# Kernel optimization log

Measured on AMD Instinct MI355X. Metric: run time of the kernel, lower is better.

Reference implementation:

```python
import jax, jax.numpy as jnp
import numpy as np

N_HEADS = 4
M = 16            # n_points (neighbors kept per voxel)
DIST = 4          # manhattan distance threshold
D_MODEL = 128
D_FFN = 256
D_CHL = 64
GRID = 96         # spatial_shape per axis
LN_EPS = 1e-5
BN_EPS = 1e-3


def setup_inputs() -> dict:
    key = jax.random.key(0)
    ks = jax.random.split(key, 24)
    N = 8192
    w = lambda k, s: jax.random.normal(k, s, jnp.float32) * 0.02
    z = lambda d: jnp.zeros((d,), jnp.float32)
    o = lambda d: jnp.ones((d,), jnp.float32)
    return {
        "features": jax.random.normal(ks[0], (N, D_CHL), jnp.float32),
        "coords": jax.random.randint(ks[1], (N, 3), 0, GRID, jnp.int32),
        "pe_w1": w(ks[2], (3, D_MODEL // 2)), "pe_b1": z(D_MODEL // 2),
        "pe_w2": w(ks[3], (D_MODEL // 2, D_MODEL)), "pe_b2": z(D_MODEL),
        "in_w": w(ks[4], (D_CHL, D_MODEL)), "in_b": z(D_MODEL),
        "q_w": w(ks[5], (D_MODEL, D_MODEL)), "q_b": z(D_MODEL),
        "k_w": w(ks[6], (D_MODEL, D_MODEL)), "k_b": z(D_MODEL),
        "v_w": w(ks[7], (D_MODEL, D_MODEL)), "v_b": z(D_MODEL),
        "o_w": w(ks[8], (D_MODEL, D_MODEL)), "o_b": z(D_MODEL),
        "n1_g": o(D_MODEL), "n1_b": z(D_MODEL),
        "l1_w": w(ks[9], (D_MODEL, D_FFN)), "l1_b": z(D_FFN),
        "l2_w": w(ks[10], (D_FFN, D_MODEL)), "l2_b": z(D_MODEL),
        "n3_g": o(D_MODEL), "n3_b": z(D_MODEL),
        "fu_w": w(ks[11], (D_MODEL + D_CHL, D_CHL)), "fu_b": z(D_CHL),
        "bn_g": o(D_CHL), "bn_b": z(D_CHL),
    }


def _layernorm(x, g, b):
    mu = jnp.mean(x, -1, keepdims=True)
    var = jnp.mean(jnp.square(x - mu), -1, keepdims=True)
    return (x - mu) * jax.lax.rsqrt(var + LN_EPS) * g + b


def reference(features, coords, pe_w1, pe_b1, pe_w2, pe_b2, in_w, in_b,
              q_w, q_b, k_w, k_b, v_w, v_b, o_w, o_b, n1_g, n1_b,
              l1_w, l1_b, l2_w, l2_b, n3_g, n3_b, fu_w, fu_b, bn_g, bn_b):
    N = features.shape[0]
    hd = D_MODEL // N_HEADS
    ci = coords.astype(jnp.float32)
    # input projection + dynamic learnable positional encoding
    src = features @ in_w + in_b
    vc = ci / (GRID - 1.0)
    src = src + (jax.nn.relu(vc @ pe_w1 + pe_b1) @ pe_w2 + pe_b2)
    # pairwise manhattan distances; accumulate per coordinate to avoid [N,N,3]
    dist = jnp.zeros((N, N), jnp.float32)
    for d in range(3):
        dist = dist + jnp.abs(ci[:, d, None] - ci[None, :, d])
    dist = jnp.where(dist <= DIST, dist, jnp.inf)
    neg_top, idx = jax.lax.top_k(-dist, M)          # [N, M]
    valid = neg_top != -jnp.inf
    # gather neighbor features; invalid slots are zero (as in torch)
    nb = jnp.where(valid[:, :, None], src[jnp.where(valid, idx, 0)], 0.0)  # [N,M,D]
    # cross-attention: query is neighbor 0 (self). NOTE: faithful raw .view
    # reshape of [N,M,D] -> [N,H,M,hd] (interleaves neighbor/head axes as torch does)
    q = (nb[:, :1] @ q_w + q_b).reshape(N, N_HEADS, 1, hd)
    k = (nb @ k_w + k_b).reshape(N, N_HEADS, M, hd)
    v = (nb @ v_w + v_b).reshape(N, N_HEADS, M, hd)
    scores = jnp.einsum('nhqd,nhkd->nhqk', q, k) / jnp.sqrt(jnp.float32(D_MODEL))
    attn = jax.nn.softmax(scores, axis=-1)
    head_out = jnp.einsum('nhqk,nhkd->nhqd', attn, v).reshape(N, D_MODEL)
    out = head_out @ o_w + o_b
    tgt = _layernorm(src + out, n1_g, n1_b)
    # FFN
    tgt2 = jax.nn.relu(tgt @ l1_w + l1_b) @ l2_w + l2_b
    tgt = _layernorm(tgt + tgt2, n3_g, n3_b)
    # EnhancedFusion: concat -> linear -> batchnorm (train-mode stats) -> relu
    fused = jnp.concatenate([features, tgt], axis=1) @ fu_w + fu_b
    mu = jnp.mean(fused, 0)
    var = jnp.var(fused, 0)
    fused = (fused - mu) * jax.lax.rsqrt(var + BN_EPS) * bn_g + bn_b
    return jax.nn.relu(fused)
```

## Files before the change

### kernel.cpp

```cpp
#include <hip/hip_runtime.h>

#define DEVFN __device__ __forceinline__

DEVFN float relu(float x) { return x < 0.f ? 0.f : x; }

typedef _Float16 h2 __attribute__((ext_vector_type(2)));
DEVFN float dot2(unsigned a, unsigned b, float c) {
    return __builtin_amdgcn_fdot2(__builtin_bit_cast(h2, a),
                                  __builtin_bit_cast(h2, b), c, false);
}
DEVFN unsigned pack2(float x, float y) {
    h2 h; h.x = (_Float16)x; h.y = (_Float16)y;
    return __builtin_bit_cast(unsigned, h);
}

#define OFF_Q   0
#define OFF_K   8192
#define OFF_V   16384
#define OFF_O   24576
#define OFF_L1  32768
#define OFF_L2  49152
#define OFF_IN  65536
#define OFF_PE  69632
#define OFF_FU  73728
#define PACKED_TOTAL 79872

__global__ __launch_bounds__(256) void k0_pack(
    const float* __restrict__ q_w, const float* __restrict__ k_w,
    const float* __restrict__ v_w, const float* __restrict__ o_w,
    const float* __restrict__ l1_w, const float* __restrict__ l2_w,
    const float* __restrict__ in_w, const float* __restrict__ pe_w2,
    const float* __restrict__ fu_w, unsigned* __restrict__ dst)
{
    const int gid = blockIdx.x * 256 + threadIdx.x;
    const int stride = gridDim.x * 256;
    auto packmat = [&](const float* s, int K, int C, unsigned* d) {
        const int kp2 = K / 2;
        const int n = kp2 * C;
        const int c4 = C * 4;
        for (int i = gid; i < n; i += stride) {
            int kp4 = i / c4;
            int rem = i - kp4 * c4;
            int c = rem >> 2, ki = rem & 3;
            int kp = kp4 * 4 + ki;
            d[i] = pack2(s[(2 * kp) * C + c], s[(2 * kp + 1) * C + c]);
        }
    };
    packmat(q_w, 128, 128, dst + OFF_Q);
    packmat(k_w, 128, 128, dst + OFF_K);
    packmat(v_w, 128, 128, dst + OFF_V);
    packmat(o_w, 128, 128, dst + OFF_O);
    packmat(l1_w, 128, 256, dst + OFF_L1);
    packmat(l2_w, 256, 128, dst + OFF_L2);
    packmat(in_w, 64, 128, dst + OFF_IN);
    packmat(pe_w2, 64, 128, dst + OFF_PE);
    packmat(fu_w, 192, 64, dst + OFF_FU);
}

__global__ __launch_bounds__(256, 4) void ka_pre_cst(
    const float* __restrict__ features, const int* __restrict__ coords,
    const float* __restrict__ pe_w1, const float* __restrict__ pe_b1,
    const float* __restrict__ pe_b2,
    const float* __restrict__ in_b,
    const unsigned* __restrict__ wH,
    float* __restrict__ src,
    float* __restrict__ qs, float* __restrict__ ks, float* __restrict__ vs,
    int* __restrict__ nbr, float* __restrict__ bnAcc, int N)
{
    __shared__ __align__(16) float S[1024];
    __shared__ __align__(16) unsigned SH[512];
    __shared__ __align__(16) unsigned FHp[256];
    __shared__ __align__(16) unsigned HHp[256];
    __shared__ int   sC[24];
    __shared__ int cnt[16];
    __shared__ int lst[16 * 64];
    __shared__ int outL[256];

    const int tid = threadIdx.x;
    const int bx = blockIdx.x;
    const int role_nbr = (bx % 3) == 2;

    if (role_nbr) {
        const int nb = bx / 3;
        const int q0 = nb * 16;
        if (nb == 0 && tid < 128) bnAcc[tid] = 0.f;
        if (tid < 16) cnt[tid] = 0;
        outL[tid] = -1;
        __syncthreads();
        int qx[16], qy[16], qz[16];
#pragma unroll
        for (int q = 0; q < 16; ++q) {
            qx[q] = coords[(q0 + q) * 3 + 0];
            qy[q] = coords[(q0 + q) * 3 + 1];
            qz[q] = coords[(q0 + q) * 3 + 2];
        }
        for (int cd = tid; cd < N; cd += 256) {
            int cx = coords[cd * 3 + 0];
            int cy = coords[cd * 3 + 1];
            int cz = coords[cd * 3 + 2];
#pragma unroll
            for (int q = 0; q < 16; ++q) {
                int dx = cx - qx[q]; dx = dx < 0 ? -dx : dx;
                int dy = cy - qy[q]; dy = dy < 0 ? -dy : dy;
                int dz = cz - qz[q]; dz = dz < 0 ? -dz : dz;
                int d = dx + dy + dz;
                if (d <= 4) {
                    int s = atomicAdd(&cnt[q], 1);
                    if (s < 64) lst[q * 64 + s] = (d << 13) | cd;
                }
            }
        }
        __syncthreads();
        {
            const int q = tid >> 4, t = tid & 15;
            int n = cnt[q]; if (n > 64) n = 64;
            for (int e = t; e < n; e += 16) {
                int key = lst[q * 64 + e];
                int rank = 0;
                for (int j = 0; j < n; ++j) rank += (lst[q * 64 + j] < key) ? 1 : 0;
                if (rank < 16) outL[q * 16 + rank] = key & 8191;
            }
        }
        __syncthreads();
        {
            const int q = tid >> 4, t = tid & 15;
            nbr[(q0 + q) * 16 + t] = outL[q * 16 + t];
        }
        return;
    }

    const int sb = (bx / 3) * 2 + (bx % 3);
    const int r0 = sb * 8;
    if (tid < 24) sC[tid] = coords[r0 * 3 + tid];
    if (tid < 256) {
        float2 f = *(const float2*)(features + r0 * 64 + tid * 2);
        FHp[tid] = pack2(f.x, f.y);
    }
    __syncthreads();
    if (tid < 256) {
        int r = tid >> 5, t2 = (tid & 31) * 2;
        float v0 = sC[r * 3 + 0] * (1.f / 95.f);
        float v1 = sC[r * 3 + 1] * (1.f / 95.f);
        float v2 = sC[r * 3 + 2] * (1.f / 95.f);
        float h0 = v0 * pe_w1[t2] + v1 * pe_w1[64 + t2] + v2 * pe_w1[128 + t2] + pe_b1[t2];
        float h1 = v0 * pe_w1[t2 + 1] + v1 * pe_w1[64 + t2 + 1] + v2 * pe_w1[128 + t2 + 1] + pe_b1[t2 + 1];
        HHp[tid] = pack2(relu(h0), relu(h1));
    }
    __syncthreads();
    const int c = tid & 127, rh = tid >> 7;
    {
        const unsigned* inH = wH + OFF_IN + c * 4;
        const unsigned* peH = wH + OFF_PE + c * 4;
        float acc[4];
        const float base = in_b[c] + pe_b2[c];
#pragma unroll
        for (int r = 0; r < 4; ++r) acc[r] = base;
        for (int kp4 = 0; kp4 < 8; ++kp4) {
            uint4 wi = *(const uint4*)(inH + kp4 * 512);
            uint4 wp = *(const uint4*)(peH + kp4 * 512);
#pragma unroll
            for (int r = 0; r < 4; ++r) {
                const int rr = rh * 4 + r;
                uint4 f = *(const uint4*)(&FHp[rr * 32 + kp4 * 4]);
                uint4 h = *(const uint4*)(&HHp[rr * 32 + kp4 * 4]);
                acc[r] = dot2(f.x, wi.x, acc[r]); acc[r] = dot2(f.y, wi.y, acc[r]);
                acc[r] = dot2(f.z, wi.z, acc[r]); acc[r] = dot2(f.w, wi.w, acc[r]);
                acc[r] = dot2(h.x, wp.x, acc[r]); acc[r] = dot2(h.y, wp.y, acc[r]);
                acc[r] = dot2(h.z, wp.z, acc[r]); acc[r] = dot2(h.w, wp.w, acc[r]);
            }
        }
#pragma unroll
        for (int r = 0; r < 4; ++r) {
            src[(r0 + rh * 4 + r) * 128 + c] = acc[r];
            S[(rh * 4 + r) * 128 + c] = acc[r];
        }
    }
    __syncthreads();
    for (int i = tid; i < 512; i += 256) {
        float2 s = *(const float2*)(&S[i * 2]);
        SH[i] = pack2(s.x, s.y);
    }
    __syncthreads();
    {
        const unsigned* qH = wH + OFF_Q + c * 4;
        const unsigned* kH = wH + OFF_K + c * 4;
        const unsigned* vH = wH + OFF_V + c * 4;
        float aq[4], ak[4], av[4];
#pragma unroll
        for (int r = 0; r < 4; ++r) { aq[r] = 0.f; ak[r] = 0.f; av[r] = 0.f; }
        for (int kp4 = 0; kp4 < 16; ++kp4) {
            uint4 wq = *(const uint4*)(qH + kp4 * 512);
            uint4 wk = *(const uint4*)(kH + kp4 * 512);
            uint4 wv = *(const uint4*)(vH + kp4 * 512);
#pragma unroll
            for (int r = 0; r < 4; ++r) {
                uint4 s4 = *(const uint4*)(&SH[(rh * 4 + r) * 64 + kp4 * 4]);
                aq[r] = dot2(s4.x, wq.x, aq[r]); aq[r] = dot2(s4.y, wq.y, aq[r]);
                aq[r] = dot2(s4.z, wq.z, aq[r]); aq[r] = dot2(s4.w, wq.w, aq[r]);
                ak[r] = dot2(s4.x, wk.x, ak[r]); ak[r] = dot2(s4.y, wk.y, ak[r]);
                ak[r] = dot2(s4.z, wk.z, ak[r]); ak[r] = dot2(s4.w, wk.w, ak[r]);
                av[r] = dot2(s4.x, wv.x, av[r]); av[r] = dot2(s4.y, wv.y, av[r]);
                av[r] = dot2(s4.z, wv.z, av[r]); av[r] = dot2(s4.w, wv.w, av[r]);
            }
        }
#pragma unroll
        for (int r = 0; r < 4; ++r) {
            qs[(r0 + rh * 4 + r) * 128 + c] = aq[r];
            ks[(r0 + rh * 4 + r) * 128 + c] = ak[r];
            vs[(r0 + rh * 4 + r) * 128 + c] = av[r];
        }
    }
}

DEVFN void ln_rows8_pack(float* Cb, unsigned* CHp, const float* __restrict__ g,
                         const float* __restrict__ b, int tid)
{
    const int r = tid >> 5, l = tid & 31;
    float x[4]; float s = 0.f, s2 = 0.f;
#pragma unroll
    for (int i = 0; i < 4; ++i) {
        x[i] = Cb[r * 128 + l * 4 + i];
        s += x[i]; s2 += x[i] * x[i];
    }
#pragma unroll
    for (int o = 1; o < 32; o <<= 1) { s += __shfl_xor(s, o); s2 += __shfl_xor(s2, o); }
    float mu = s * (1.f / 128.f);
    float var = s2 * (1.f / 128.f) - mu * mu;
    float rstd = rsqrtf(var + 1e-5f);
    float y[4];
#pragma unroll
    for (int i = 0; i < 4; ++i) {
        int cc = l * 4 + i;
        y[i] = (x[i] - mu) * rstd * g[cc] + b[cc];
        Cb[r * 128 + cc] = y[i];
    }
    CHp[r * 64 + l * 2]     = pack2(y[0], y[1]);
    CHp[r * 64 + l * 2 + 1] = pack2(y[2], y[3]);
}

__global__ __launch_bounds__(256, 4) void k4_main_cst(
    const float* __restrict__ features, const float* __restrict__ src,
    const float* __restrict__ qs, const float* __restrict__ ks, const float* __restrict__ vs,
    const int* __restrict__ nbr,
    const float* __restrict__ q_b, const float* __restrict__ k_b,
    const float* __restrict__ v_b,
    const unsigned* __restrict__ wH,
    const float* __restrict__ o_b,
    const float* __restrict__ n1_g, const float* __restrict__ n1_b,
    const float* __restrict__ l1_b,
    const float* __restrict__ l2_b,
    const float* __restrict__ n3_g, const float* __restrict__ n3_b,
    const float* __restrict__ fu_b,
    float* __restrict__ fused, float* __restrict__ bnSum, float* __restrict__ bnSq)
{
    __shared__ __align__(16) float A[1024];
    __shared__ __align__(16) float C[1024];
    __shared__ __align__(16) float Q[1024];
    __shared__ __align__(16) float SC[512];
    __shared__ __align__(16) unsigned BtH[512];
    __shared__ __align__(16) unsigned CH[512];
    __shared__ __align__(16) unsigned FH[256];
    __shared__ __align__(16) _Float16 Hh[2048];
    __shared__ __align__(16) float bK[128], bV[128];
    __shared__ int idxL[128];
    const int tid = threadIdx.x;
    const int r0 = blockIdx.x * 8;

    for (int i = tid; i < 1024; i += 256) A[i] = src[r0 * 128 + i];
    if (tid < 256) {
        float2 f = *(const float2*)(features + r0 * 64 + tid * 2);
        FH[tid] = pack2(f.x, f.y);
    }
    if (tid < 128) {
        idxL[tid] = nbr[r0 * 16 + tid];
        bK[tid] = k_b[tid]; bV[tid] = v_b[tid];
    }
    __syncthreads();
    {
        int r = tid >> 5, cg = tid & 31;
        int i0 = idxL[r * 16];
        float4 qv = make_float4(0.f, 0.f, 0.f, 0.f);
        if (i0 >= 0) qv = *(const float4*)(qs + i0 * 128 + cg * 4);
        float4 qb = *(const float4*)(q_b + cg * 4);
        qv.x += qb.x; qv.y += qb.y; qv.z += qb.z; qv.w += qb.w;
        *(float4*)(&Q[r * 128 + cg * 4]) = qv;
    }
    __syncthreads();

    const int ar = tid >> 5, ah = (tid >> 3) & 3, ag = tid & 7;
    {
        const int ch = ag & 3;
        float sbias = 0.f;
#pragma unroll
        for (int c4 = 0; c4 < 8; ++c4) {
            float4 qv = *(const float4*)(&Q[ar * 128 + ah * 32 + c4 * 4]);
            float4 kb = *(const float4*)(&bK[ch * 32 + c4 * 4]);
            sbias += qv.x * kb.x + qv.y * kb.y + qv.z * kb.z + qv.w * kb.w;
        }
#pragma unroll
        for (int jj = 0; jj < 2; ++jj) {
            int j = ag + jj * 8;
            int j4 = j >> 2;
            int id = idxL[ar * 16 + ah * 4 + j4];
            float s = 0.f;
            if (id >= 0) {
#pragma unroll
                for (int c4 = 0; c4 < 8; ++c4) {
                    float4 qv = *(const float4*)(&Q[ar * 128 + ah * 32 + c4 * 4]);
                    float4 kv = *(const float4*)(ks + id * 128 + ch * 32 + c4 * 4);
                    s += qv.x * kv.x + qv.y * kv.y + qv.z * kv.z + qv.w * kv.w;
                }
            }
            SC[ar * 64 + ah * 16 + j] = (s + sbias) * 0.08838834764831845f;
        }
    }
    __syncthreads();

    {
        float p[16];
        float mx = -3.4e38f;
#pragma unroll
        for (int j = 0; j < 16; ++j) { p[j] = SC[ar * 64 + ah * 16 + j]; mx = fmaxf(mx, p[j]); }
        float sum = 0.f;
#pragma unroll
        for (int j = 0; j < 16; ++j) { p[j] = __expf(p[j] - mx); sum += p[j]; }
        float inv = 1.f / sum;
        float4 acc = make_float4(0.f, 0.f, 0.f, 0.f);
#pragma unroll
        for (int j = 0; j < 16; ++j) {
            int j4 = j >> 2, ch = j & 3;
            int id = idxL[ar * 16 + ah * 4 + j4];
            float w = p[j] * inv;
            if (id >= 0) {
                float4 vv = *(const float4*)(vs + id * 128 + ch * 32 + ag * 4);
                acc.x += w * vv.x; acc.y += w * vv.y;
                acc.z += w * vv.z; acc.w += w * vv.w;
            }
        }
        float4 vb = *(const float4*)(&bV[ah * 32 + ag * 4]);
        acc.x += vb.x; acc.y += vb.y; acc.z += vb.z; acc.w += vb.w;
        BtH[ar * 64 + ah * 16 + ag * 2]     = pack2(acc.x, acc.y);
        BtH[ar * 64 + ah * 16 + ag * 2 + 1] = pack2(acc.z, acc.w);
    }
    __syncthreads();

    {
        const int c = tid & 127, rh = tid >> 7;
        const unsigned* oH = wH + OFF_O + c * 4;
        float acc[4];
#pragma unroll
        for (int r = 0; r < 4; ++r) acc[r] = 0.f;
        for (int kp4 = 0; kp4 < 16; ++kp4) {
            uint4 w = *(const uint4*)(oH + kp4 * 512);
#pragma unroll
            for (int r = 0; r < 4; ++r) {
                uint4 t = *(const uint4*)(&BtH[(rh * 4 + r) * 64 + kp4 * 4]);
                acc[r] = dot2(t.x, w.x, acc[r]); acc[r] = dot2(t.y, w.y, acc[r]);
                acc[r] = dot2(t.z, w.z, acc[r]); acc[r] = dot2(t.w, w.w, acc[r]);
            }
        }
        const float ob = o_b[c];
#pragma unroll
        for (int r = 0; r < 4; ++r) {
            const int rr = rh * 4 + r;
            C[rr * 128 + c] = A[rr * 128 + c] + ob + acc[r];
        }
    }
    __syncthreads();
    ln_rows8_pack(C, CH, n1_g, n1_b, tid);
    __syncthreads();

    {
        const int f = tid;
        const unsigned* l1H = wH + OFF_L1 + f * 4;
        float acc[8];
#pragma unroll
        for (int r = 0; r < 8; ++r) acc[r] = 0.f;
        for (int kp4 = 0; kp4 < 16; ++kp4) {
            uint4 w = *(const uint4*)(l1H + kp4 * 1024);
#pragma unroll
            for (int r = 0; r < 8; ++r) {
                uint4 t = *(const uint4*)(&CH[r * 64 + kp4 * 4]);
                acc[r] = dot2(t.x, w.x, acc[r]); acc[r] = dot2(t.y, w.y, acc[r]);
                acc[r] = dot2(t.z, w.z, acc[r]); acc[r] = dot2(t.w, w.w, acc[r]);
            }
        }
        const float bb = l1_b[f];
#pragma unroll
        for (int r = 0; r < 8; ++r) Hh[r * 256 + f] = (_Float16)relu(acc[r] + bb);
    }
    __syncthreads();
    {
    }

    {
        const int c = tid & 127, rh = tid >> 7;
        const unsigned* l2H = wH + OFF_L2 + c * 4;
        const unsigned* HhU = (const unsigned*)Hh;
        float acc[4];
#pragma unroll
        for (int r = 0; r < 4; ++r) acc[r] = 0.f;
        for (int kp4 = 0; kp4 < 32; ++kp4) {
            uint4 w = *(const uint4*)(l2H + kp4 * 512);
#pragma unroll
            for (int r = 0; r < 4; ++r) {
                uint4 t = *(const uint4*)(&HhU[(rh * 4 + r) * 128 + kp4 * 4]);
                acc[r] = dot2(t.x, w.x, acc[r]); acc[r] = dot2(t.y, w.y, acc[r]);
                acc[r] = dot2(t.z, w.z, acc[r]); acc[r] = dot2(t.w, w.w, acc[r]);
            }
        }
        const float lb = l2_b[c];
#pragma unroll
        for (int r = 0; r < 4; ++r) {
            const int rr = rh * 4 + r;
            C[rr * 128 + c] += lb + acc[r];
        }
    }
    __syncthreads();
    ln_rows8_pack(C, CH, n3_g, n3_b, tid);
    __syncthreads();

    {
        const int c = tid & 63, rg = tid >> 6;
        const unsigned* fuH = wH + OFF_FU + c * 4;
        float acc[2];
        const float fb = fu_b[c];
#pragma unroll
        for (int r = 0; r < 2; ++r) acc[r] = fb;
        for (int kp4 = 0; kp4 < 8; ++kp4) {
            uint4 w = *(const uint4*)(fuH + kp4 * 256);
#pragma unroll
            for (int r = 0; r < 2; ++r) {
                uint4 t = *(const uint4*)(&FH[(rg * 2 + r) * 32 + kp4 * 4]);
                acc[r] = dot2(t.x, w.x, acc[r]); acc[r] = dot2(t.y, w.y, acc[r]);
                acc[r] = dot2(t.z, w.z, acc[r]); acc[r] = dot2(t.w, w.w, acc[r]);
            }
        }
        for (int kp4 = 0; kp4 < 16; ++kp4) {
            uint4 w = *(const uint4*)(fuH + (8 + kp4) * 256);
#pragma unroll
            for (int r = 0; r < 2; ++r) {
                uint4 t = *(const uint4*)(&CH[(rg * 2 + r) * 64 + kp4 * 4]);
                acc[r] = dot2(t.x, w.x, acc[r]); acc[r] = dot2(t.y, w.y, acc[r]);
                acc[r] = dot2(t.z, w.z, acc[r]); acc[r] = dot2(t.w, w.w, acc[r]);
            }
        }
#pragma unroll
        for (int r = 0; r < 2; ++r) {
            int row = rg * 2 + r;
            float v = acc[r];
            fused[(r0 + row) * 64 + c] = v;
            A[row * 64 + c] = v;
        }
    }
    __syncthreads();
    if (tid < 64) {
        float s = 0.f, s2 = 0.f;
#pragma unroll
        for (int r = 0; r < 8; ++r) { float x = A[r * 64 + tid]; s += x; s2 += x * x; }
        atomicAdd(&bnSum[tid], s);
        atomicAdd(&bnSq[tid], s2);
    }
}

__global__ __launch_bounds__(256) void k5_bn_cst(
    const float* __restrict__ fused, const float* __restrict__ bnSum,
    const float* __restrict__ bnSq,
    const float* __restrict__ g, const float* __restrict__ b,
    float* __restrict__ out, int N)
{
    const int total = N * 64;
    const float invN = 1.f / (float)N;
    for (int i = blockIdx.x * 256 + threadIdx.x; i < total; i += gridDim.x * 256) {
        int c = i & 63;
        float mu = bnSum[c] * invN;
        float var = bnSq[c] * invN - mu * mu;
        float x = fused[i];
        float y = (x - mu) * rsqrtf(var + 1e-3f) * g[c] + b[c];
        out[i] = relu(y);
    }
}

extern "C" void kernel_launch(void* const* d_in, const int* in_sizes, int n_in,
                              void* d_out, int out_size, void* d_ws, size_t ws_size,
                              hipStream_t stream)
{
    const float* features = (const float*)d_in[0];
    const int*   coords   = (const int*)d_in[1];
    const float* pe_w1 = (const float*)d_in[2];
    const float* pe_b1 = (const float*)d_in[3];
    const float* pe_w2 = (const float*)d_in[4];
    const float* pe_b2 = (const float*)d_in[5];
    const float* in_w  = (const float*)d_in[6];
    const float* in_b  = (const float*)d_in[7];
    const float* q_w   = (const float*)d_in[8];
    const float* q_b   = (const float*)d_in[9];
    const float* k_w   = (const float*)d_in[10];
    const float* k_b   = (const float*)d_in[11];
    const float* v_w   = (const float*)d_in[12];
    const float* v_b   = (const float*)d_in[13];
    const float* o_w   = (const float*)d_in[14];
    const float* o_b   = (const float*)d_in[15];
    const float* n1_g  = (const float*)d_in[16];
    const float* n1_b  = (const float*)d_in[17];
    const float* l1_w  = (const float*)d_in[18];
    const float* l1_b  = (const float*)d_in[19];
    const float* l2_w  = (const float*)d_in[20];
    const float* l2_b  = (const float*)d_in[21];
    const float* n3_g  = (const float*)d_in[22];
    const float* n3_b  = (const float*)d_in[23];
    const float* fu_w  = (const float*)d_in[24];
    const float* fu_b  = (const float*)d_in[25];
    const float* bn_g  = (const float*)d_in[26];
    const float* bn_b  = (const float*)d_in[27];

    const int N = in_sizes[0] / 64;

    float* src   = (float*)d_ws;
    float* qs    = src + (size_t)N * 128;
    float* ks    = qs  + (size_t)N * 128;
    float* vs    = ks  + (size_t)N * 128;
    float* fused = vs  + (size_t)N * 128;
    int*   nbr    = (int*)(fused + (size_t)N * 64);
    float* bnSum  = (float*)(nbr + (size_t)N * 16);
    float* bnSq   = bnSum + 64;
    unsigned* wH  = (unsigned*)(bnSq + 64);

    k0_pack<<<64, 256, 0, stream>>>(q_w, k_w, v_w, o_w, l1_w, l2_w,
                                    in_w, pe_w2, fu_w, wH);
    ka_pre_cst<<<N / 8 + N / 16, 256, 0, stream>>>(features, coords,
                                                   pe_w1, pe_b1, pe_b2, in_b,
                                                   wH,
                                                   src, qs, ks, vs, nbr, bnSum, N);
    k4_main_cst<<<N / 8, 256, 0, stream>>>(features, src, qs, ks, vs, nbr,
                                           q_b, k_b, v_b, wH, o_b, n1_g, n1_b,
                                           l1_b, l2_b, n3_g, n3_b,
                                           fu_b, fused, bnSum, bnSq);
    k5_bn_cst<<<512, 256, 0, stream>>>(fused, bnSum, bnSq, bn_g, bn_b,
                                       (float*)d_out, N);
}
```

Baseline: 207.6 us.

## Fuse all stages into one cooperative persistent kernel with grid syncs

Replaces the four launches (weight pack, pre-projection/neighbor search, main attention+FFN, batchnorm) with one cooperative kernel of N/16 blocks. Each block handles two 8-row tiles, separated by grid.sync barriers. The src activations and fused outputs stay in registers across phases instead of going to global memory, and shared memory is a union across phases. This removes launch overhead and intermediate global traffic, at the cost of grid-wide barriers and 512 blocks that must all be co-resident. If the cooperative launch fails, the old kernels run instead.

```diff
diff --git a/kernel.cpp b/kernel.cpp
--- a/kernel.cpp
+++ b/kernel.cpp
@@ -1,4 +1,7 @@
 #include <hip/hip_runtime.h>
+#include <hip/hip_cooperative_groups.h>
+
+namespace cg = cooperative_groups;
 
 #define DEVFN __device__ __forceinline__
 
@@ -23,7 +26,481 @@
 #define OFF_IN  65536
 #define OFF_PE  69632
 #define OFF_FU  73728
-#define PACKED_TOTAL 79872
+
+struct MegaParams {
+    const float* features; const int* coords;
+    const float* pe_w1; const float* pe_b1; const float* pe_w2; const float* pe_b2;
+    const float* in_w;  const float* in_b;
+    const float* q_w;   const float* q_b;
+    const float* k_w;   const float* k_b;
+    const float* v_w;   const float* v_b;
+    const float* o_w;   const float* o_b;
+    const float* n1_g;  const float* n1_b;
+    const float* l1_w;  const float* l1_b;
+    const float* l2_w;  const float* l2_b;
+    const float* n3_g;  const float* n3_b;
+    const float* fu_w;  const float* fu_b;
+    const float* bn_g;  const float* bn_b;
+    float* qs; float* ks; float* vs; int* nbr;
+    float* bnSum; float* bnSq; unsigned* wH;
+    float* out; int N;
+};
+
+__global__ __launch_bounds__(256, 2) void mega_cst(MegaParams P)
+{
+    cg::grid_group grid = cg::this_grid();
+    const int tid = threadIdx.x;
+    const int bx = blockIdx.x;
+    const int gid = bx * 256 + tid;
+
+    __shared__ union SU {
+        struct {
+            float S[1024];
+            unsigned SH[512];
+            unsigned FHp[256];
+            unsigned HHp[256];
+            int sC[24];
+            int cnt[8];
+            int lst[8 * 64];
+            int outL[128];
+        } ka;
+        struct {
+            float A[1024]; float C[1024]; float Q[1024]; float SC[512];
+            unsigned BtH[512]; unsigned CH[512]; unsigned FH[256];
+            _Float16 Hh[2048]; float bK[128]; float bV[128]; int idxL[128];
+        } k4;
+    } U;
+
+    {
+        const int stride = gridDim.x * 256;
+        auto packmat = [&](const float* s, int K, int C, unsigned* d) {
+            const int kp2 = K / 2;
+            const int n = kp2 * C;
+            const int c4 = C * 4;
+            for (int i = gid; i < n; i += stride) {
+                int kp4 = i / c4;
+                int rem = i - kp4 * c4;
+                int c = rem >> 2, ki = rem & 3;
+                int kp = kp4 * 4 + ki;
+                d[i] = pack2(s[(2 * kp) * C + c], s[(2 * kp + 1) * C + c]);
+            }
+        };
+        packmat(P.q_w, 128, 128, P.wH + OFF_Q);
+        packmat(P.k_w, 128, 128, P.wH + OFF_K);
+        packmat(P.v_w, 128, 128, P.wH + OFF_V);
+        packmat(P.o_w, 128, 128, P.wH + OFF_O);
+        packmat(P.l1_w, 128, 256, P.wH + OFF_L1);
+        packmat(P.l2_w, 256, 128, P.wH + OFF_L2);
+        packmat(P.in_w, 64, 128, P.wH + OFF_IN);
+        packmat(P.pe_w2, 64, 128, P.wH + OFF_PE);
+        packmat(P.fu_w, 192, 64, P.wH + OFF_FU);
+        if (gid < 128) P.bnSum[gid] = 0.f;
+    }
+    __threadfence();
+    grid.sync();
+
+    float accS[2][4];
+
+#pragma unroll
+    for (int t = 0; t < 2; ++t) {
+        const int r0 = (bx + t * 512) * 8;
+        __syncthreads();
+
+        if (tid < 24) U.ka.sC[tid] = P.coords[r0 * 3 + tid];
+        {
+            float2 f = *(const float2*)(P.features + r0 * 64 + tid * 2);
+            U.ka.FHp[tid] = pack2(f.x, f.y);
+        }
+        __syncthreads();
+        {
+            int r = tid >> 5, t2 = (tid & 31) * 2;
+            float v0 = U.ka.sC[r * 3 + 0] * (1.f / 95.f);
+            float v1 = U.ka.sC[r * 3 + 1] * (1.f / 95.f);
+            float v2 = U.ka.sC[r * 3 + 2] * (1.f / 95.f);
+            float h0 = v0 * P.pe_w1[t2] + v1 * P.pe_w1[64 + t2] + v2 * P.pe_w1[128 + t2] + P.pe_b1[t2];
+            float h1 = v0 * P.pe_w1[t2 + 1] + v1 * P.pe_w1[64 + t2 + 1] + v2 * P.pe_w1[128 + t2 + 1] + P.pe_b1[t2 + 1];
+            U.ka.HHp[tid] = pack2(relu(h0), relu(h1));
+        }
+        __syncthreads();
+        const int c = tid & 127, rh = tid >> 7;
+        {
+            const unsigned* inH = P.wH + OFF_IN + c * 4;
+            const unsigned* peH = P.wH + OFF_PE + c * 4;
+            float acc[4];
+            const float base = P.in_b[c] + P.pe_b2[c];
+#pragma unroll
+            for (int r = 0; r < 4; ++r) acc[r] = base;
+            for (int kp4 = 0; kp4 < 8; ++kp4) {
+                uint4 wi = *(const uint4*)(inH + kp4 * 512);
+                uint4 wp = *(const uint4*)(peH + kp4 * 512);
+#pragma unroll
+                for (int r = 0; r < 4; ++r) {
+                    const int rr = rh * 4 + r;
+                    uint4 f = *(const uint4*)(&U.ka.FHp[rr * 32 + kp4 * 4]);
+                    uint4 h = *(const uint4*)(&U.ka.HHp[rr * 32 + kp4 * 4]);
+                    acc[r] = dot2(f.x, wi.x, acc[r]); acc[r] = dot2(f.y, wi.y, acc[r]);
+                    acc[r] = dot2(f.z, wi.z, acc[r]); acc[r] = dot2(f.w, wi.w, acc[r]);
+                    acc[r] = dot2(h.x, wp.x, acc[r]); acc[r] = dot2(h.y, wp.y, acc[r]);
+                    acc[r] = dot2(h.z, wp.z, acc[r]); acc[r] = dot2(h.w, wp.w, acc[r]);
+                }
+            }
+#pragma unroll
+            for (int r = 0; r < 4; ++r) {
+                U.ka.S[(rh * 4 + r) * 128 + c] = acc[r];
+                accS[t][r] = acc[r];
+            }
+        }
+        __syncthreads();
+        for (int i = tid; i < 512; i += 256) {
+            float2 s = *(const float2*)(&U.ka.S[i * 2]);
+            U.ka.SH[i] = pack2(s.x, s.y);
+        }
+        __syncthreads();
+        {
+            const unsigned* qH = P.wH + OFF_Q + c * 4;
+            const unsigned* kH = P.wH + OFF_K + c * 4;
+            const unsigned* vH = P.wH + OFF_V + c * 4;
+            float aq[4], ak[4], av[4];
+#pragma unroll
+            for (int r = 0; r < 4; ++r) { aq[r] = 0.f; ak[r] = 0.f; av[r] = 0.f; }
+            for (int kp4 = 0; kp4 < 16; ++kp4) {
+                uint4 wq = *(const uint4*)(qH + kp4 * 512);
+                uint4 wk = *(const uint4*)(kH + kp4 * 512);
+                uint4 wv = *(const uint4*)(vH + kp4 * 512);
+#pragma unroll
+                for (int r = 0; r < 4; ++r) {
+                    uint4 s4 = *(const uint4*)(&U.ka.SH[(rh * 4 + r) * 64 + kp4 * 4]);
+                    aq[r] = dot2(s4.x, wq.x, aq[r]); aq[r] = dot2(s4.y, wq.y, aq[r]);
+                    aq[r] = dot2(s4.z, wq.z, aq[r]); aq[r] = dot2(s4.w, wq.w, aq[r]);
+                    ak[r] = dot2(s4.x, wk.x, ak[r]); ak[r] = dot2(s4.y, wk.y, ak[r]);
+                    ak[r] = dot2(s4.z, wk.z, ak[r]); ak[r] = dot2(s4.w, wk.w, ak[r]);
+                    av[r] = dot2(s4.x, wv.x, av[r]); av[r] = dot2(s4.y, wv.y, av[r]);
+                    av[r] = dot2(s4.z, wv.z, av[r]); av[r] = dot2(s4.w, wv.w, av[r]);
+                }
+            }
+#pragma unroll
+            for (int r = 0; r < 4; ++r) {
+                P.qs[(r0 + rh * 4 + r) * 128 + c] = aq[r];
+                P.ks[(r0 + rh * 4 + r) * 128 + c] = ak[r];
+                P.vs[(r0 + rh * 4 + r) * 128 + c] = av[r];
+            }
+        }
+
+        if (tid < 8) U.ka.cnt[tid] = 0;
+        if (tid < 128) U.ka.outL[tid] = -1;
+        __syncthreads();
+        {
+            int qx[8], qy[8], qz[8];
+#pragma unroll
+            for (int q = 0; q < 8; ++q) {
+                qx[q] = P.coords[(r0 + q) * 3 + 0];
+                qy[q] = P.coords[(r0 + q) * 3 + 1];
+                qz[q] = P.coords[(r0 + q) * 3 + 2];
+            }
+            for (int cd = tid; cd < P.N; cd += 256) {
+                int cx = P.coords[cd * 3 + 0];
+                int cy = P.coords[cd * 3 + 1];
+                int cz = P.coords[cd * 3 + 2];
+#pragma unroll
+                for (int q = 0; q < 8; ++q) {
+                    int dx = cx - qx[q]; dx = dx < 0 ? -dx : dx;
+                    int dy = cy - qy[q]; dy = dy < 0 ? -dy : dy;
+                    int dz = cz - qz[q]; dz = dz < 0 ? -dz : dz;
+                    int d = dx + dy + dz;
+                    if (d <= 4) {
+                        int s = atomicAdd(&U.ka.cnt[q], 1);
+                        if (s < 64) U.ka.lst[q * 64 + s] = (d << 13) | cd;
+                    }
+                }
+            }
+        }
+        __syncthreads();
+        {
+            const int q = tid >> 5, tt = tid & 31;
+            int n = U.ka.cnt[q]; if (n > 64) n = 64;
+            for (int e = tt; e < n; e += 32) {
+                int key = U.ka.lst[q * 64 + e];
+                int rank = 0;
+                for (int j = 0; j < n; ++j) rank += (U.ka.lst[q * 64 + j] < key) ? 1 : 0;
+                if (rank < 16) U.ka.outL[q * 16 + rank] = key & 8191;
+            }
+        }
+        __syncthreads();
+        if (tid < 128) {
+            int q = tid >> 4, tt = tid & 15;
+            P.nbr[(r0 + q) * 16 + tt] = U.ka.outL[tid];
+        }
+    }
+    __threadfence();
+    grid.sync();
+
+    float accF[2][2];
+
+#pragma unroll
+    for (int t = 0; t < 2; ++t) {
+        const int r0 = (bx + t * 512) * 8;
+        __syncthreads();
+
+#pragma unroll
+        for (int r = 0; r < 4; ++r)
+            U.k4.A[((tid >> 7) * 4 + r) * 128 + (tid & 127)] = accS[t][r];
+        {
+            float2 f = *(const float2*)(P.features + r0 * 64 + tid * 2);
+            U.k4.FH[tid] = pack2(f.x, f.y);
+        }
+        if (tid < 128) {
+            U.k4.idxL[tid] = P.nbr[r0 * 16 + tid];
+            U.k4.bK[tid] = P.k_b[tid]; U.k4.bV[tid] = P.v_b[tid];
+        }
+        __syncthreads();
+        {
+            int r = tid >> 5, cg2 = tid & 31;
+            int i0 = U.k4.idxL[r * 16];
+            float4 qv = make_float4(0.f, 0.f, 0.f, 0.f);
+            if (i0 >= 0) qv = *(const float4*)(P.qs + i0 * 128 + cg2 * 4);
+            float4 qb = *(const float4*)(P.q_b + cg2 * 4);
+            qv.x += qb.x; qv.y += qb.y; qv.z += qb.z; qv.w += qb.w;
+            *(float4*)(&U.k4.Q[r * 128 + cg2 * 4]) = qv;
+        }
+        __syncthreads();
+
+        const int ar = tid >> 5, ah = (tid >> 3) & 3, ag = tid & 7;
+        {
+            const int ch = ag & 3;
+            float sbias = 0.f;
+#pragma unroll
+            for (int c4 = 0; c4 < 8; ++c4) {
+                float4 qv = *(const float4*)(&U.k4.Q[ar * 128 + ah * 32 + c4 * 4]);
+                float4 kb = *(const float4*)(&U.k4.bK[ch * 32 + c4 * 4]);
+                sbias += qv.x * kb.x + qv.y * kb.y + qv.z * kb.z + qv.w * kb.w;
+            }
+#pragma unroll
+            for (int jj = 0; jj < 2; ++jj) {
+                int j = ag + jj * 8;
+                int j4 = j >> 2;
+                int id = U.k4.idxL[ar * 16 + ah * 4 + j4];
+                float s = 0.f;
+                if (id >= 0) {
+#pragma unroll
+                    for (int c4 = 0; c4 < 8; ++c4) {
+                        float4 qv = *(const float4*)(&U.k4.Q[ar * 128 + ah * 32 + c4 * 4]);
+                        float4 kv = *(const float4*)(P.ks + id * 128 + ch * 32 + c4 * 4);
+                        s += qv.x * kv.x + qv.y * kv.y + qv.z * kv.z + qv.w * kv.w;
+                    }
+                }
+                U.k4.SC[ar * 64 + ah * 16 + j] = (s + sbias) * 0.08838834764831845f;
+            }
+        }
+        __syncthreads();
+
+        {
+            float p[16];
+            float mx = -3.4e38f;
+#pragma unroll
+            for (int j = 0; j < 16; ++j) { p[j] = U.k4.SC[ar * 64 + ah * 16 + j]; mx = fmaxf(mx, p[j]); }
+            float sum = 0.f;
+#pragma unroll
+            for (int j = 0; j < 16; ++j) { p[j] = __expf(p[j] - mx); sum += p[j]; }
+            float inv = 1.f / sum;
+            float4 acc = make_float4(0.f, 0.f, 0.f, 0.f);
+#pragma unroll
+            for (int j = 0; j < 16; ++j) {
+                int j4 = j >> 2, ch = j & 3;
+                int id = U.k4.idxL[ar * 16 + ah * 4 + j4];
+                float w = p[j] * inv;
+                if (id >= 0) {
+                    float4 vv = *(const float4*)(P.vs + id * 128 + ch * 32 + ag * 4);
+                    acc.x += w * vv.x; acc.y += w * vv.y;
+                    acc.z += w * vv.z; acc.w += w * vv.w;
+                }
+            }
+            float4 vb = *(const float4*)(&U.k4.bV[ah * 32 + ag * 4]);
+            acc.x += vb.x; acc.y += vb.y; acc.z += vb.z; acc.w += vb.w;
+            U.k4.BtH[ar * 64 + ah * 16 + ag * 2]     = pack2(acc.x, acc.y);
+            U.k4.BtH[ar * 64 + ah * 16 + ag * 2 + 1] = pack2(acc.z, acc.w);
+        }
+        __syncthreads();
+
+        {
+            const int c = tid & 127, rh = tid >> 7;
+            const unsigned* oH = P.wH + OFF_O + c * 4;
+            float acc[4];
+#pragma unroll
+            for (int r = 0; r < 4; ++r) acc[r] = 0.f;
+            for (int kp4 = 0; kp4 < 16; ++kp4) {
+                uint4 w = *(const uint4*)(oH + kp4 * 512);
+#pragma unroll
+                for (int r = 0; r < 4; ++r) {
+                    uint4 tt = *(const uint4*)(&U.k4.BtH[(rh * 4 + r) * 64 + kp4 * 4]);
+                    acc[r] = dot2(tt.x, w.x, acc[r]); acc[r] = dot2(tt.y, w.y, acc[r]);
+                    acc[r] = dot2(tt.z, w.z, acc[r]); acc[r] = dot2(tt.w, w.w, acc[r]);
+                }
+            }
+            const float ob = P.o_b[c];
+#pragma unroll
+            for (int r = 0; r < 4; ++r) {
+                const int rr = rh * 4 + r;
+                U.k4.C[rr * 128 + c] = U.k4.A[rr * 128 + c] + ob + acc[r];
+            }
+        }
+        __syncthreads();
+        {
+            const int r = tid >> 5, l = tid & 31;
+            float x[4]; float s = 0.f, s2 = 0.f;
+#pragma unroll
+            for (int i = 0; i < 4; ++i) {
+                x[i] = U.k4.C[r * 128 + l * 4 + i];
+                s += x[i]; s2 += x[i] * x[i];
+            }
+#pragma unroll
+            for (int o = 1; o < 32; o <<= 1) { s += __shfl_xor(s, o); s2 += __shfl_xor(s2, o); }
+            float mu = s * (1.f / 128.f);
+            float var = s2 * (1.f / 128.f) - mu * mu;
+            float rstd = rsqrtf(var + 1e-5f);
+            float y[4];
+#pragma unroll
+            for (int i = 0; i < 4; ++i) {
+                int cc = l * 4 + i;
+                y[i] = (x[i] - mu) * rstd * P.n1_g[cc] + P.n1_b[cc];
+                U.k4.C[r * 128 + cc] = y[i];
+            }
+            U.k4.CH[r * 64 + l * 2]     = pack2(y[0], y[1]);
+            U.k4.CH[r * 64 + l * 2 + 1] = pack2(y[2], y[3]);
+        }
+        __syncthreads();
+
+        {
+            const int f = tid;
+            const unsigned* l1H = P.wH + OFF_L1 + f * 4;
+            float acc[8];
+#pragma unroll
+            for (int r = 0; r < 8; ++r) acc[r] = 0.f;
+            for (int kp4 = 0; kp4 < 16; ++kp4) {
+                uint4 w = *(const uint4*)(l1H + kp4 * 1024);
+#pragma unroll
+                for (int r = 0; r < 8; ++r) {
+                    uint4 tt = *(const uint4*)(&U.k4.CH[r * 64 + kp4 * 4]);
+                    acc[r] = dot2(tt.x, w.x, acc[r]); acc[r] = dot2(tt.y, w.y, acc[r]);
+                    acc[r] = dot2(tt.z, w.z, acc[r]); acc[r] = dot2(tt.w, w.w, acc[r]);
+                }
+            }
+            const float bb = P.l1_b[f];
+#pragma unroll
+            for (int r = 0; r < 8; ++r) U.k4.Hh[r * 256 + f] = (_Float16)relu(acc[r] + bb);
+        }
+        __syncthreads();
+
+        {
+            const int c = tid & 127, rh = tid >> 7;
+            const unsigned* l2H = P.wH + OFF_L2 + c * 4;
+            const unsigned* HhU = (const unsigned*)U.k4.Hh;
+            float acc[4];
+#pragma unroll
+            for (int r = 0; r < 4; ++r) acc[r] = 0.f;
+            for (int kp4 = 0; kp4 < 32; ++kp4) {
+                uint4 w = *(const uint4*)(l2H + kp4 * 512);
+#pragma unroll
+                for (int r = 0; r < 4; ++r) {
+                    uint4 tt = *(const uint4*)(&HhU[(rh * 4 + r) * 128 + kp4 * 4]);
+                    acc[r] = dot2(tt.x, w.x, acc[r]); acc[r] = dot2(tt.y, w.y, acc[r]);
+                    acc[r] = dot2(tt.z, w.z, acc[r]); acc[r] = dot2(tt.w, w.w, acc[r]);
+                }
+            }
+            const float lb = P.l2_b[c];
+#pragma unroll
+            for (int r = 0; r < 4; ++r) {
+                const int rr = rh * 4 + r;
+                U.k4.C[rr * 128 + c] += lb + acc[r];
+            }
+        }
+        __syncthreads();
+        {
+            const int r = tid >> 5, l = tid & 31;
+            float x[4]; float s = 0.f, s2 = 0.f;
+#pragma unroll
+            for (int i = 0; i < 4; ++i) {
+                x[i] = U.k4.C[r * 128 + l * 4 + i];
+                s += x[i]; s2 += x[i] * x[i];
+            }
+#pragma unroll
+            for (int o = 1; o < 32; o <<= 1) { s += __shfl_xor(s, o); s2 += __shfl_xor(s2, o); }
+            float mu = s * (1.f / 128.f);
+            float var = s2 * (1.f / 128.f) - mu * mu;
+            float rstd = rsqrtf(var + 1e-5f);
+            float y[4];
+#pragma unroll
+            for (int i = 0; i < 4; ++i) {
+                int cc = l * 4 + i;
+                y[i] = (x[i] - mu) * rstd * P.n3_g[cc] + P.n3_b[cc];
+                U.k4.C[r * 128 + cc] = y[i];
+            }
+            U.k4.CH[r * 64 + l * 2]     = pack2(y[0], y[1]);
+            U.k4.CH[r * 64 + l * 2 + 1] = pack2(y[2], y[3]);
+        }
+        __syncthreads();
+
+        {
+            const int c = tid & 63, rg = tid >> 6;
+            const unsigned* fuH = P.wH + OFF_FU + c * 4;
+            float acc[2];
+            const float fb = P.fu_b[c];
+#pragma unroll
+            for (int r = 0; r < 2; ++r) acc[r] = fb;
+            for (int kp4 = 0; kp4 < 8; ++kp4) {
+                uint4 w = *(const uint4*)(fuH + kp4 * 256);
+#pragma unroll
+                for (int r = 0; r < 2; ++r) {
+                    uint4 tt = *(const uint4*)(&U.k4.FH[(rg * 2 + r) * 32 + kp4 * 4]);
+                    acc[r] = dot2(tt.x, w.x, acc[r]); acc[r] = dot2(tt.y, w.y, acc[r]);
+                    acc[r] = dot2(tt.z, w.z, acc[r]); acc[r] = dot2(tt.w, w.w, acc[r]);
+                }
+            }
+            for (int kp4 = 0; kp4 < 16; ++kp4) {
+                uint4 w = *(const uint4*)(fuH + (8 + kp4) * 256);
+#pragma unroll
+                for (int r = 0; r < 2; ++r) {
+                    uint4 tt = *(const uint4*)(&U.k4.CH[(rg * 2 + r) * 64 + kp4 * 4]);
+                    acc[r] = dot2(tt.x, w.x, acc[r]); acc[r] = dot2(tt.y, w.y, acc[r]);
+                    acc[r] = dot2(tt.z, w.z, acc[r]); acc[r] = dot2(tt.w, w.w, acc[r]);
+                }
+            }
+#pragma unroll
+            for (int r = 0; r < 2; ++r) {
+                int row = rg * 2 + r;
+                U.k4.A[row * 64 + c] = acc[r];
+                accF[t][r] = acc[r];
+            }
+        }
+        __syncthreads();
+        if (tid < 64) {
+            float s = 0.f, s2 = 0.f;
+#pragma unroll
+            for (int r = 0; r < 8; ++r) { float x = U.k4.A[r * 64 + tid]; s += x; s2 += x * x; }
+            atomicAdd(&P.bnSum[tid], s);
+            atomicAdd(&P.bnSq[tid], s2);
+        }
+    }
+    __threadfence();
+    grid.sync();
+
+    {
+        const int c = tid & 63, rg = tid >> 6;
+        const float invN = 1.f / (float)P.N;
+        float mu = P.bnSum[c] * invN;
+        float var = P.bnSq[c] * invN - mu * mu;
+        float rstd = rsqrtf(var + 1e-3f);
+        float gg = P.bn_g[c], bb = P.bn_b[c];
+#pragma unroll
+        for (int t = 0; t < 2; ++t) {
+            const int r0 = (bx + t * 512) * 8;
+#pragma unroll
+            for (int r = 0; r < 2; ++r) {
+                float y = (accF[t][r] - mu) * rstd * gg + bb;
+                P.out[(r0 + rg * 2 + r) * 64 + c] = relu(y);
+            }
+        }
+    }
+}
 
 __global__ __launch_bounds__(256) void k0_pack(
     const float* __restrict__ q_w, const float* __restrict__ k_w,
@@ -390,8 +867,6 @@
         for (int r = 0; r < 8; ++r) Hh[r * 256 + f] = (_Float16)relu(acc[r] + bb);
     }
     __syncthreads();
-    {
-    }
 
     {
         const int c = tid & 127, rh = tid >> 7;
@@ -485,57 +960,57 @@
                               void* d_out, int out_size, void* d_ws, size_t ws_size,
                               hipStream_t stream)
 {
-    const float* features = (const float*)d_in[0];
-    const int*   coords   = (const int*)d_in[1];
-    const float* pe_w1 = (const float*)d_in[2];
-    const float* pe_b1 = (const float*)d_in[3];
-    const float* pe_w2 = (const float*)d_in[4];
-    const float* pe_b2 = (const float*)d_in[5];
-    const float* in_w  = (const float*)d_in[6];
-    const float* in_b  = (const float*)d_in[7];
-    const float* q_w   = (const float*)d_in[8];
-    const float* q_b   = (const float*)d_in[9];
-    const float* k_w   = (const float*)d_in[10];
-    const float* k_b   = (const float*)d_in[11];
-    const float* v_w   = (const float*)d_in[12];
-    const float* v_b   = (const float*)d_in[13];
-    const float* o_w   = (const float*)d_in[14];
-    const float* o_b   = (const float*)d_in[15];
-    const float* n1_g  = (const float*)d_in[16];
-    const float* n1_b  = (const float*)d_in[17];
-    const float* l1_w  = (const float*)d_in[18];
-    const float* l1_b  = (const float*)d_in[19];
-    const float* l2_w  = (const float*)d_in[20];
-    const float* l2_b  = (const float*)d_in[21];
-    const float* n3_g  = (const float*)d_in[22];
-    const float* n3_b  = (const float*)d_in[23];
-    const float* fu_w  = (const float*)d_in[24];
-    const float* fu_b  = (const float*)d_in[25];
-    const float* bn_g  = (const float*)d_in[26];
-    const float* bn_b  = (const float*)d_in[27];
-
     const int N = in_sizes[0] / 64;
 
     float* src   = (float*)d_ws;
     float* qs    = src + (size_t)N * 128;
-    float* ks    = qs  + (size_t)N * 128;
-    float* vs    = ks  + (size_t)N * 128;
-    float* fused = vs  + (size_t)N * 128;
-    int*   nbr    = (int*)(fused + (size_t)N * 64);
-    float* bnSum  = (float*)(nbr + (size_t)N * 16);
-    float* bnSq   = bnSum + 64;
-    unsigned* wH  = (unsigned*)(bnSq + 64);
-
-    k0_pack<<<64, 256, 0, stream>>>(q_w, k_w, v_w, o_w, l1_w, l2_w,
-                                    in_w, pe_w2, fu_w, wH);
-    ka_pre_cst<<<N / 8 + N / 16, 256, 0, stream>>>(features, coords,
-                                                   pe_w1, pe_b1, pe_b2, in_b,
-                                                   wH,
-                                                   src, qs, ks, vs, nbr, bnSum, N);
-    k4_main_cst<<<N / 8, 256, 0, stream>>>(features, src, qs, ks, vs, nbr,
-                                           q_b, k_b, v_b, wH, o_b, n1_g, n1_b,
-                                           l1_b, l2_b, n3_g, n3_b,
-                                           fu_b, fused, bnSum, bnSq);
-    k5_bn_cst<<<512, 256, 0, stream>>>(fused, bnSum, bnSq, bn_g, bn_b,
-                                       (float*)d_out, N);
+    float* ks    = qs + (size_t)N * 128;
+    float* vs    = ks + (size_t)N * 128;
+    float* fused = vs + (size_t)N * 128;
+    int*   nbr   = (int*)(fused + (size_t)N * 64);
+    float* bnSum = (float*)(nbr + (size_t)N * 16);
+    float* bnSq  = bnSum + 64;
+    unsigned* wH = (unsigned*)(bnSq + 64);
+
+    MegaParams P;
+    P.features = (const float*)d_in[0];
+    P.coords   = (const int*)d_in[1];
+    P.pe_w1 = (const float*)d_in[2];  P.pe_b1 = (const float*)d_in[3];
+    P.pe_w2 = (const float*)d_in[4];  P.pe_b2 = (const float*)d_in[5];
+    P.in_w  = (const float*)d_in[6];  P.in_b  = (const float*)d_in[7];
+    P.q_w   = (const float*)d_in[8];  P.q_b   = (const float*)d_in[9];
+    P.k_w   = (const float*)d_in[10]; P.k_b   = (const float*)d_in[11];
+    P.v_w   = (const float*)d_in[12]; P.v_b   = (const float*)d_in[13];
+    P.o_w   = (const float*)d_in[14]; P.o_b   = (const float*)d_in[15];
+    P.n1_g  = (const float*)d_in[16]; P.n1_b  = (const float*)d_in[17];
+    P.l1_w  = (const float*)d_in[18]; P.l1_b  = (const float*)d_in[19];
+    P.l2_w  = (const float*)d_in[20]; P.l2_b  = (const float*)d_in[21];
+    P.n3_g  = (const float*)d_in[22]; P.n3_b  = (const float*)d_in[23];
+    P.fu_w  = (const float*)d_in[24]; P.fu_b  = (const float*)d_in[25];
+    P.bn_g  = (const float*)d_in[26]; P.bn_b  = (const float*)d_in[27];
+    P.qs = qs; P.ks = ks; P.vs = vs; P.nbr = nbr;
+    P.bnSum = bnSum; P.bnSq = bnSq; P.wH = wH;
+    P.out = (float*)d_out; P.N = N;
+
+    void* args[] = { (void*)&P };
+    hipError_t err = hipLaunchCooperativeKernel((const void*)mega_cst,
+                                                dim3(N / 16), dim3(256),
+                                                args, 0, stream);
+    if (err != hipSuccess) {
+        k0_pack<<<64, 256, 0, stream>>>(P.q_w, P.k_w, P.v_w, P.o_w,
+                                        P.l1_w, P.l2_w, P.in_w, P.pe_w2,
+                                        P.fu_w, wH);
+        ka_pre_cst<<<N / 8 + N / 16, 256, 0, stream>>>(P.features, P.coords,
+                                                       P.pe_w1, P.pe_b1, P.pe_b2,
+                                                       P.in_b, wH,
+                                                       src, qs, ks, vs, nbr,
+                                                       bnSum, N);
+        k4_main_cst<<<N / 8, 256, 0, stream>>>(P.features, src, qs, ks, vs, nbr,
+                                               P.q_b, P.k_b, P.v_b, wH, P.o_b,
+                                               P.n1_g, P.n1_b, P.l1_b, P.l2_b,
+                                               P.n3_g, P.n3_b, P.fu_b,
+                                               fused, bnSum, bnSq);
+        k5_bn_cst<<<512, 256, 0, stream>>>(fused, bnSum, bnSq, P.bn_g, P.bn_b,
+                                           (float*)d_out, N);
+    }
 }
```

Measured after the change: 551.5 us. 166% more time.
